# Kernel tuning notes

Measured on AMD Instinct MI355X. Metric: run time of the kernel, lower is better.

Reference implementation:

```python
import jax, jax.numpy as jnp
from jax import lax
import numpy as np

TOP_K = 2
CAPACITY_FACTOR = 1.0


def setup_inputs() -> dict:
    key = jax.random.key(0)
    kx, kg, k1, k2 = jax.random.split(key, 4)
    B, S, D, F, E = 8, 4096, 512, 1024, 16
    x = jax.random.normal(kx, (B, S, D), dtype=jnp.float32)
    w_gate = jax.random.normal(kg, (D, E), dtype=jnp.float32) * 0.02
    w1 = jax.random.normal(k1, (E, D, 2 * F), dtype=jnp.float32) * 0.02
    w2 = jax.random.normal(k2, (E, F, D), dtype=jnp.float32) * 0.02
    return {"x": x, "w_gate": w_gate, "w1": w1, "w2": w2}


def reference(x, w_gate, w1, w2):
    # Inference mode: no gating noise, dropout is identity.
    B, S, D = x.shape
    E = w_gate.shape[1]
    T = B * S
    capacity = max(1, int(CAPACITY_FACTOR * T / E))  # static

    flat = x.reshape(T, D)
    gate_logits = flat @ w_gate                      # [T, E]
    gate_scores = jax.nn.softmax(gate_logits, axis=-1)
    topk_vals, topk_idx = lax.top_k(gate_scores, TOP_K)  # [T, k]

    phi_mean = gate_scores.mean(axis=0)
    aux_loss = E * jnp.sum(phi_mean * phi_mean)

    # Per-expert combine weight for every token: [E, T]
    onehot = topk_idx[None, :, :] == jnp.arange(E)[:, None, None]  # [E, T, k]
    w_et = jnp.sum(jnp.where(onehot, topk_vals[None], 0.0), axis=-1)  # [E, T]

    # Capacity truncation: keep the `capacity` highest-weight tokens per expert
    sel_w, sel_idx = lax.top_k(w_et, capacity)  # [E, C]; unrouted picks have weight 0

    xs = flat[sel_idx]                                  # [E, C, D] gather
    h = jnp.einsum('ecd,edf->ecf', xs, w1)              # [E, C, 2F]
    h1, h2 = jnp.split(h, 2, axis=-1)
    act = h1 * jax.nn.silu(h2)                          # SwiGLU
    out_e = jnp.einsum('ecf,efd->ecd', act, w2) * sel_w[..., None]  # [E, C, D]

    combined = jnp.zeros((T, D), dtype=flat.dtype).at[sel_idx.reshape(-1)].add(
        out_e.reshape(-1, D))
    return combined.reshape(B, S, D), aux_loss
```

## Files before the change

### kernel.cpp

```cpp
#include <hip/hip_runtime.h>
#include <hip/hip_bf16.h>
#include <math.h>

#define T_TOK 32768
#define D_DIM 512
#define E_EXP 16
#define F_DIM 1024
#define C_CAP 2048

typedef __attribute__((ext_vector_type(8))) __bf16 bf16x8;
typedef __attribute__((ext_vector_type(4))) float f32x4;

__device__ __forceinline__ unsigned short f2bf(float f) {
  unsigned u = __float_as_uint(f);
  u += 0x7FFFu + ((u >> 16) & 1u);
  return (unsigned short)(u >> 16);
}

__device__ __forceinline__ void gld16(const void* gptr, void* ldsptr) {
  __builtin_amdgcn_global_load_lds(
      (__attribute__((address_space(1))) void*)(void*)gptr,
      (__attribute__((address_space(3))) void*)ldsptr, 16, 0, 0);
}

__global__ void transpose_conv_kernel(const float* __restrict__ in,
                                      unsigned short* __restrict__ out,
                                      int R, int Cc) {
  __shared__ float tile[32][33];
  int e = blockIdx.z;
  int r0 = blockIdx.y * 32, c0 = blockIdx.x * 32;
  const float* pin = in + (size_t)e * R * Cc;
  unsigned short* pout = out + (size_t)e * R * Cc;
  int tx = threadIdx.x, ty = threadIdx.y;
  #pragma unroll
  for (int i = 0; i < 32; i += 8)
    tile[ty + i][tx] = pin[(size_t)(r0 + ty + i) * Cc + c0 + tx];
  __syncthreads();
  #pragma unroll
  for (int i = 0; i < 32; i += 8)
    pout[(size_t)(c0 + ty + i) * R + r0 + tx] = f2bf(tile[tx][ty + i]);
}

__global__ __launch_bounds__(256) void gate_kernel(
    const float* __restrict__ x, const float* __restrict__ wg,
    float* __restrict__ w_et, float* __restrict__ phi_sum,
    unsigned short* __restrict__ xb) {
  __shared__ float wgl[D_DIM * E_EXP];
  __shared__ float phil[E_EXP];
  int tid = threadIdx.x;
  for (int i = tid; i < D_DIM * E_EXP; i += 256) wgl[i] = wg[i];
  if (tid < E_EXP) phil[tid] = 0.f;
  __syncthreads();

  int g = tid >> 4;
  int e = tid & 15;
  int t = blockIdx.x * 16 + g;

  float acc = 0.f;
  const float* xr = x + (size_t)t * D_DIM;
  #pragma unroll 4
  for (int d = 0; d < D_DIM; d += 4) {
    float4 xv = *(const float4*)(xr + d);
    acc = fmaf(xv.x, wgl[(d + 0) * 16 + e], acc);
    acc = fmaf(xv.y, wgl[(d + 1) * 16 + e], acc);
    acc = fmaf(xv.z, wgl[(d + 2) * 16 + e], acc);
    acc = fmaf(xv.w, wgl[(d + 3) * 16 + e], acc);
  }

  unsigned short* xrow = xb + (size_t)t * D_DIM;
  #pragma unroll
  for (int j = 0; j < 8; ++j) {
    int idx = j * 16 + e;
    float4 v = *(const float4*)(xr + idx * 4);
    ushort4 o;
    o.x = f2bf(v.x); o.y = f2bf(v.y); o.z = f2bf(v.z); o.w = f2bf(v.w);
    ((ushort4*)xrow)[idx] = o;
  }

  float m = acc;
  for (int off = 8; off; off >>= 1) m = fmaxf(m, __shfl_xor(m, off));
  float p = expf(acc - m);
  float s = p;
  for (int off = 8; off; off >>= 1) s += __shfl_xor(s, off);
  float score = p / s;
  atomicAdd(&phil[e], score);

  float v1 = score; int i1 = e;
  for (int off = 8; off; off >>= 1) {
    float ov = __shfl_xor(v1, off); int oi = __shfl_xor(i1, off);
    if (ov > v1 || (ov == v1 && oi < i1)) { v1 = ov; i1 = oi; }
  }
  float sc2 = (e == i1) ? -1.f : score;
  float v2 = sc2; int i2 = e;
  for (int off = 8; off; off >>= 1) {
    float ov = __shfl_xor(v2, off); int oi = __shfl_xor(i2, off);
    if (ov > v2 || (ov == v2 && oi < i2)) { v2 = ov; i2 = oi; }
  }
  if (e == 0) {
    w_et[(size_t)i1 * T_TOK + t] = v1;
    w_et[(size_t)i2 * T_TOK + t] = v2;
  }
  __syncthreads();
  if (tid < E_EXP) atomicAdd(&phi_sum[tid], phil[tid]);
}

__global__ void aux_kernel(const float* __restrict__ phi_sum, float* __restrict__ out_aux) {
  if (threadIdx.x == 0) {
    float s = 0.f;
    for (int e = 0; e < E_EXP; ++e) {
      float pm = phi_sum[e] / (float)T_TOK;
      s += pm * pm;
    }
    *out_aux = (float)E_EXP * s;
  }
}

template<int P>
__global__ __launch_bounds__(256) void s_hist(
    const float* __restrict__ w_et, unsigned* __restrict__ hist,
    const unsigned* __restrict__ prefix, const unsigned* __restrict__ done) {
  int c = blockIdx.x, e = blockIdx.y, tid = threadIdx.x;
  if (P > 0 && done[e]) return;
  __shared__ unsigned lh[2048];
  for (int i = tid; i < 2048; i += 256) lh[i] = 0;
  __syncthreads();
  const float* w = w_et + (size_t)e * T_TOK + c * 2048;
  unsigned pfx = (P > 0) ? prefix[e] : 0u;
  #pragma unroll
  for (int i = 0; i < 8; ++i) {
    unsigned b = __float_as_uint(w[i * 256 + tid]);
    if (P == 0) { if (b) atomicAdd(&lh[b >> 21], 1u); }
    else if (P == 1) { if ((b >> 21) == (pfx >> 21)) atomicAdd(&lh[(b >> 10) & 0x7FFu], 1u); }
    else { if ((b >> 10) == (pfx >> 10)) atomicAdd(&lh[b & 0x3FFu], 1u); }
  }
  __syncthreads();
  for (int i = tid; i < 2048; i += 256)
    if (lh[i]) atomicAdd(&hist[e * 2048 + i], lh[i]);
}

template<int P>
__global__ __launch_bounds__(1024) void s_pick(
    const unsigned* __restrict__ hist, unsigned* __restrict__ prefix,
    unsigned* __restrict__ krem, unsigned* __restrict__ done) {
  int tid = threadIdx.x, lane = tid & 63, e = tid >> 6;
  if (P > 0 && done[e]) return;
  const int BPL = (P == 2) ? 16 : 32;
  const int SH = (P == 0) ? 21 : (P == 1) ? 10 : 0;
  const unsigned* h = hist + e * 2048;
  unsigned S = 0;
  for (int i = 0; i < BPL; ++i) S += h[lane * BPL + i];
  unsigned U = S;
  #pragma unroll
  for (int off = 1; off < 64; off <<= 1) {
    unsigned t = __shfl_down(U, off);
    if (lane + off < 64) U += t;
  }
  unsigned Unext = __shfl_down(U, 1);
  if (lane == 63) Unext = 0;
  unsigned k = (P == 0) ? (unsigned)C_CAP : krem[e];
  if (P == 0 && lane == 0) {
    if (U < k) { done[e] = 1; prefix[e] = 0; krem[e] = 0; }
    else done[e] = 0;
  }
  if (U >= k && Unext < k) {
    unsigned cum = Unext; int chosen = 0; unsigned knew = 0;
    for (int i = BPL - 1; i >= 0; --i) {
      unsigned hh = h[lane * BPL + i];
      if (cum + hh >= k) { chosen = lane * BPL + i; knew = k - cum; break; }
      cum += hh;
    }
    if (P == 0) prefix[e] = ((unsigned)chosen) << SH;
    else prefix[e] = prefix[e] | (((unsigned)chosen) << SH);
    krem[e] = knew;
  }
}

__global__ __launch_bounds__(256) void s_count(
    const float* __restrict__ w_et, const unsigned* __restrict__ prefix,
    unsigned* __restrict__ cnt) {
  int c = blockIdx.x, e = blockIdx.y, tid = threadIdx.x;
  unsigned thr = prefix[e];
  const uint4* up = (const uint4*)(w_et + (size_t)e * T_TOK + c * 2048 + tid * 8);
  uint4 va = up[0], vb = up[1];
  unsigned gt = 0, eq = 0;
  unsigned vals[8] = {va.x, va.y, va.z, va.w, vb.x, vb.y, vb.z, vb.w};
  #pragma unroll
  for (int i = 0; i < 8; ++i) {
    if (vals[i] > thr) gt++;
    else if (vals[i] == thr) eq++;
  }
  __shared__ unsigned sc[256];
  sc[tid] = (gt << 16) | eq;
  __syncthreads();
  for (int s = 128; s; s >>= 1) {
    if (tid < s) sc[tid] += sc[tid + s];
    __syncthreads();
  }
  if (tid == 0) cnt[e * 16 + c] = sc[0];
}

__global__ __launch_bounds__(64) void s_base(
    const unsigned* __restrict__ cnt, unsigned* __restrict__ gbase,
    unsigned* __restrict__ ebase, unsigned* __restrict__ gtt,
    unsigned* __restrict__ eqt) {
  int e = threadIdx.x;
  if (e >= 16) return;
  unsigned g = 0, q = 0;
  #pragma unroll
  for (int c = 0; c < 16; ++c) {
    unsigned p = cnt[e * 16 + c];
    gbase[e * 16 + c] = g;
    ebase[e * 16 + c] = q;
    g += p >> 16;
    q += p & 0xFFFFu;
  }
  gtt[e] = g;
  eqt[e] = (unsigned)C_CAP - g;
}

__global__ __launch_bounds__(256) void s_write(
    const float* __restrict__ w_et, const unsigned* __restrict__ prefix,
    const unsigned* __restrict__ gbase, const unsigned* __restrict__ ebase,
    const unsigned* __restrict__ gtt, const unsigned* __restrict__ eqt,
    int* __restrict__ sel_idx, float* __restrict__ sel_w) {
  int c = blockIdx.x, e = blockIdx.y, tid = threadIdx.x;
  unsigned thr = prefix[e];
  const uint4* up = (const uint4*)(w_et + (size_t)e * T_TOK + c * 2048 + tid * 8);
  uint4 va = up[0], vb = up[1];
  unsigned vals[8] = {va.x, va.y, va.z, va.w, vb.x, vb.y, vb.z, vb.w};
  unsigned gt = 0, eq = 0;
  #pragma unroll
  for (int i = 0; i < 8; ++i) {
    if (vals[i] > thr) gt++;
    else if (vals[i] == thr) eq++;
  }
  __shared__ unsigned sc[256];
  unsigned mine = (gt << 16) | eq;
  sc[tid] = mine;
  __syncthreads();
  for (int off = 1; off < 256; off <<= 1) {
    unsigned add = (tid >= off) ? sc[tid - off] : 0u;
    __syncthreads();
    sc[tid] += add;
    __syncthreads();
  }
  unsigned excl = sc[tid] - mine;
  unsigned gpos = gbase[e * 16 + c] + (excl >> 16);
  unsigned qpos = ebase[e * 16 + c] + (excl & 0xFFFFu);
  unsigned gtotal = gtt[e], eqtake = eqt[e];
  int* si = sel_idx + (size_t)e * C_CAP;
  float* sw = sel_w + (size_t)e * C_CAP;
  int tokbase = c * 2048 + tid * 8;
  #pragma unroll
  for (int i = 0; i < 8; ++i) {
    unsigned b = vals[i];
    if (b > thr) {
      si[gpos] = tokbase + i; sw[gpos] = __uint_as_float(b); gpos++;
    } else if (b == thr && qpos < eqtake) {
      si[gtotal + qpos] = tokbase + i; sw[gtotal + qpos] = __uint_as_float(b); qpos++;
    }
  }
}


#define PIPE_BARRIER() do { __builtin_amdgcn_s_barrier(); __builtin_amdgcn_sched_barrier(0); } while (0)

__global__ __launch_bounds__(256, 3) void gemm1_kernel(
    const unsigned short* __restrict__ xb,
    const unsigned short* __restrict__ w1t,
    const int* __restrict__ sel_idx,
    unsigned short* __restrict__ act) {
  __shared__ __align__(16) unsigned short As[3 * 4096];
  __shared__ __align__(16) unsigned short Bs[3 * 4096];
  int bid = (blockIdx.x & 7) * 512 + (blockIdx.x >> 3);
  int nt = bid & 15, mt = (bid >> 4) & 15, e = bid >> 8;
  int tid = threadIdx.x, lane = tid & 63, wid = tid >> 6;
  int wr = wid >> 1, wc = wid & 1;
  int cl = lane & 15, rg = lane >> 4;

  int c0 = tid, c1 = 256 + tid;
  int r0 = c0 >> 2, gk0 = (c0 & 3) ^ ((r0 >> 1) & 3);
  int r1 = c1 >> 2, gk1 = (c1 & 3) ^ ((r1 >> 1) & 3);
  int tok0 = sel_idx[e * C_CAP + mt * 128 + r0];
  int tok1 = sel_idx[e * C_CAP + mt * 128 + r1];
  const unsigned short* ag0 = xb + (size_t)tok0 * D_DIM + gk0 * 8;
  const unsigned short* ag1 = xb + (size_t)tok1 * D_DIM + gk1 * 8;
  int hcol0 = (r0 < 64) ? (nt * 64 + r0) : (F_DIM + nt * 64 + (r0 - 64));
  int hcol1 = (r1 < 64) ? (nt * 64 + r1) : (F_DIM + nt * 64 + (r1 - 64));
  const unsigned short* bg0 = w1t + ((size_t)e * 2 * F_DIM + hcol0) * D_DIM + gk0 * 8;
  const unsigned short* bg1 = w1t + ((size_t)e * 2 * F_DIM + hcol1) * D_DIM + gk1 * 8;
  char* Ab = (char*)As;
  char* Bb = (char*)Bs;

#define G1_STAGE(buf, kt) do { \
    gld16(ag0 + (kt) * 32, Ab + (buf) * 8192 + tid * 16); \
    gld16(ag1 + (kt) * 32, Ab + (buf) * 8192 + 4096 + tid * 16); \
    gld16(bg0 + (kt) * 32, Bb + (buf) * 8192 + tid * 16); \
    gld16(bg1 + (kt) * 32, Bb + (buf) * 8192 + 4096 + tid * 16); \
  } while (0)

  f32x4 zero = {0.f, 0.f, 0.f, 0.f};
  f32x4 acc[4][4];
  #pragma unroll
  for (int m = 0; m < 4; ++m)
    #pragma unroll
    for (int n = 0; n < 4; ++n) acc[m][n] = zero;

#define G1_COMPUTE(buf) do { \
    const unsigned short* Ap = As + (buf) * 4096; \
    const unsigned short* Bp = Bs + (buf) * 4096; \
    bf16x8 av[4], bv[4]; \
    _Pragma("unroll") \
    for (int m = 0; m < 4; ++m) { \
      int ra = wr * 64 + m * 16 + cl; \
      av[m] = *(const bf16x8*)&Ap[(ra * 4 + (rg ^ ((ra >> 1) & 3))) * 8]; \
    } \
    _Pragma("unroll") \
    for (int n = 0; n < 4; ++n) { \
      int rb = ((n < 2) ? (wc * 32 + n * 16) : (64 + wc * 32 + (n - 2) * 16)) + cl; \
      bv[n] = *(const bf16x8*)&Bp[(rb * 4 + (rg ^ ((rb >> 1) & 3))) * 8]; \
    } \
    _Pragma("unroll") \
    for (int m = 0; m < 4; ++m) \
      _Pragma("unroll") \
      for (int n = 0; n < 4; ++n) \
        acc[m][n] = __builtin_amdgcn_mfma_f32_16x16x32_bf16(av[m], bv[n], acc[m][n], 0, 0, 0); \
  } while (0)

  const int NK = D_DIM / 32;
  G1_STAGE(0, 0);
  G1_STAGE(1, 1);
  int bc = 0, bs = 2;
  for (int kt = 0; kt < NK - 1; ++kt) {
    asm volatile("s_waitcnt vmcnt(4)" ::: "memory");
    PIPE_BARRIER();
    if (kt + 2 < NK) { G1_STAGE(bs, kt + 2); bs = (bs == 2) ? 0 : bs + 1; }
    __builtin_amdgcn_sched_barrier(0);
    G1_COMPUTE(bc);
    bc = (bc == 2) ? 0 : bc + 1;
  }
  asm volatile("s_waitcnt vmcnt(0)" ::: "memory");
  PIPE_BARRIER();
  G1_COMPUTE(bc);

  #pragma unroll
  for (int m = 0; m < 4; ++m) {
    #pragma unroll
    for (int n = 0; n < 2; ++n) {
      #pragma unroll
      for (int r = 0; r < 4; ++r) {
        int row = mt * 128 + wr * 64 + m * 16 + rg * 4 + r;
        int col = nt * 64 + wc * 32 + n * 16 + cl;
        float h1 = acc[m][n][r];
        float h2 = acc[m][n + 2][r];
        float sg = h2 / (1.f + __expf(-h2));
        act[((size_t)e * C_CAP + row) * F_DIM + col] = f2bf(h1 * sg);
      }
    }
  }
#undef G1_STAGE
#undef G1_COMPUTE
}

__global__ __launch_bounds__(256, 3) void gemm2_kernel(
    const unsigned short* __restrict__ act,
    const unsigned short* __restrict__ w2t,
    const int* __restrict__ sel_idx,
    const float* __restrict__ sel_w,
    float* __restrict__ out) {
  __shared__ __align__(16) unsigned short As[3 * 4096];
  __shared__ __align__(16) unsigned short Bs[3 * 4096];
  int bid = (blockIdx.x & 7) * 128 + (blockIdx.x >> 3);
  int nt = bid & 3, mt = (bid >> 2) & 15, e = bid >> 6;
  int tid = threadIdx.x, lane = tid & 63, wid = tid >> 6;
  int wr = wid >> 1, wc = wid & 1;
  int cl = lane & 15, rg = lane >> 4;

  int c0 = tid, c1 = 256 + tid;
  int r0 = c0 >> 2, gk0 = (c0 & 3) ^ ((r0 >> 1) & 3);
  int r1 = c1 >> 2, gk1 = (c1 & 3) ^ ((r1 >> 1) & 3);
  const unsigned short* ag0 = act + ((size_t)e * C_CAP + mt * 128 + r0) * F_DIM + gk0 * 8;
  const unsigned short* ag1 = act + ((size_t)e * C_CAP + mt * 128 + r1) * F_DIM + gk1 * 8;
  const unsigned short* bg0 = w2t + ((size_t)e * D_DIM + nt * 128 + r0) * F_DIM + gk0 * 8;
  const unsigned short* bg1 = w2t + ((size_t)e * D_DIM + nt * 128 + r1) * F_DIM + gk1 * 8;
  char* Ab = (char*)As;
  char* Bb = (char*)Bs;

#define G2_STAGE(buf, kt) do { \
    gld16(ag0 + (kt) * 32, Ab + (buf) * 8192 + tid * 16); \
    gld16(ag1 + (kt) * 32, Ab + (buf) * 8192 + 4096 + tid * 16); \
    gld16(bg0 + (kt) * 32, Bb + (buf) * 8192 + tid * 16); \
    gld16(bg1 + (kt) * 32, Bb + (buf) * 8192 + 4096 + tid * 16); \
  } while (0)

  f32x4 zero = {0.f, 0.f, 0.f, 0.f};
  f32x4 acc[4][4];
  #pragma unroll
  for (int m = 0; m < 4; ++m)
    #pragma unroll
    for (int n = 0; n < 4; ++n) acc[m][n] = zero;

#define G2_COMPUTE(buf) do { \
    const unsigned short* Ap = As + (buf) * 4096; \
    const unsigned short* Bp = Bs + (buf) * 4096; \
    bf16x8 av[4], bv[4]; \
    _Pragma("unroll") \
    for (int m = 0; m < 4; ++m) { \
      int ra = wr * 64 + m * 16 + cl; \
      av[m] = *(const bf16x8*)&Ap[(ra * 4 + (rg ^ ((ra >> 1) & 3))) * 8]; \
    } \
    _Pragma("unroll") \
    for (int n = 0; n < 4; ++n) { \
      int rb = wc * 64 + n * 16 + cl; \
      bv[n] = *(const bf16x8*)&Bp[(rb * 4 + (rg ^ ((rb >> 1) & 3))) * 8]; \
    } \
    _Pragma("unroll") \
    for (int m = 0; m < 4; ++m) \
      _Pragma("unroll") \
      for (int n = 0; n < 4; ++n) \
        acc[m][n] = __builtin_amdgcn_mfma_f32_16x16x32_bf16(av[m], bv[n], acc[m][n], 0, 0, 0); \
  } while (0)

  const int NK = F_DIM / 32;
  G2_STAGE(0, 0);
  G2_STAGE(1, 1);
  int bc = 0, bs = 2;
  for (int kt = 0; kt < NK - 1; ++kt) {
    asm volatile("s_waitcnt vmcnt(4)" ::: "memory");
    PIPE_BARRIER();
    if (kt + 2 < NK) { G2_STAGE(bs, kt + 2); bs = (bs == 2) ? 0 : bs + 1; }
    __builtin_amdgcn_sched_barrier(0);
    G2_COMPUTE(bc);
    bc = (bc == 2) ? 0 : bc + 1;
  }
  asm volatile("s_waitcnt vmcnt(0)" ::: "memory");
  PIPE_BARRIER();
  G2_COMPUTE(bc);

  #pragma unroll
  for (int m = 0; m < 4; ++m) {
    #pragma unroll
    for (int r = 0; r < 4; ++r) {
      int slot = mt * 128 + wr * 64 + m * 16 + rg * 4 + r;
      float wgt = sel_w[e * C_CAP + slot];
      int tok = sel_idx[e * C_CAP + slot];
      float* orow = out + (size_t)tok * D_DIM;
      #pragma unroll
      for (int n = 0; n < 4; ++n) {
        int col = nt * 128 + wc * 64 + n * 16 + cl;
        atomicAdd(&orow[col], acc[m][n][r] * wgt);
      }
    }
  }
#undef G2_STAGE
#undef G2_COMPUTE
}

extern "C" void kernel_launch(void* const* d_in, const int* in_sizes, int n_in,
                              void* d_out, int out_size, void* d_ws, size_t ws_size,
                              hipStream_t stream) {
  const float* x  = (const float*)d_in[0];
  const float* wg = (const float*)d_in[1];
  const float* w1 = (const float*)d_in[2];
  const float* w2 = (const float*)d_in[3];
  float* out = (float*)d_out;

  char* ws = (char*)d_ws;
  size_t off = 0;
  auto carve = [&](size_t bytes) -> void* {
    void* p = ws + off;
    off += (bytes + 255) & ~(size_t)255;
    return p;
  };
  float* w_et            = (float*)carve((size_t)E_EXP * T_TOK * 4);
  float* phi             = (float*)carve(64);
  int* sel_i             = (int*)carve((size_t)E_EXP * C_CAP * 4);
  float* sel_wv          = (float*)carve((size_t)E_EXP * C_CAP * 4);
  unsigned short* xb     = (unsigned short*)carve((size_t)T_TOK * D_DIM * 2);
  unsigned short* w1t    = (unsigned short*)carve((size_t)E_EXP * 2 * F_DIM * D_DIM * 2);
  unsigned short* w2t    = (unsigned short*)carve((size_t)E_EXP * D_DIM * F_DIM * 2);
  unsigned short* actb   = (unsigned short*)carve((size_t)E_EXP * C_CAP * F_DIM * 2);
  unsigned* hist0        = (unsigned*)carve((size_t)E_EXP * 2048 * 4);
  unsigned* hist1        = (unsigned*)carve((size_t)E_EXP * 2048 * 4);
  unsigned* hist2        = (unsigned*)carve((size_t)E_EXP * 2048 * 4);
  unsigned* prefix       = (unsigned*)carve(64 * 4);
  unsigned* krem         = (unsigned*)carve(64 * 4);
  unsigned* done         = (unsigned*)carve(64 * 4);
  unsigned* cnt          = (unsigned*)carve(256 * 4);
  unsigned* gbase        = (unsigned*)carve(256 * 4);
  unsigned* ebase        = (unsigned*)carve(256 * 4);
  unsigned* gtt          = (unsigned*)carve(64 * 4);
  unsigned* eqt          = (unsigned*)carve(64 * 4);
  if (off > ws_size) return;

  hipMemsetAsync(w_et, 0, (size_t)E_EXP * T_TOK * 4, stream);
  hipMemsetAsync(phi, 0, 64, stream);
  hipMemsetAsync(hist0, 0, (size_t)E_EXP * 2048 * 4 * 3, stream);
  hipMemsetAsync(d_out, 0, (size_t)out_size * 4, stream);

  transpose_conv_kernel<<<dim3(2 * F_DIM / 32, D_DIM / 32, E_EXP), dim3(32, 8), 0, stream>>>(
      w1, w1t, D_DIM, 2 * F_DIM);
  transpose_conv_kernel<<<dim3(D_DIM / 32, F_DIM / 32, E_EXP), dim3(32, 8), 0, stream>>>(
      w2, w2t, F_DIM, D_DIM);
  gate_kernel<<<T_TOK / 16, 256, 0, stream>>>(x, wg, w_et, phi, xb);

  s_hist<0><<<dim3(16, 16), 256, 0, stream>>>(w_et, hist0, prefix, done);
  s_pick<0><<<1, 1024, 0, stream>>>(hist0, prefix, krem, done);
  s_hist<1><<<dim3(16, 16), 256, 0, stream>>>(w_et, hist1, prefix, done);
  s_pick<1><<<1, 1024, 0, stream>>>(hist1, prefix, krem, done);
  s_hist<2><<<dim3(16, 16), 256, 0, stream>>>(w_et, hist2, prefix, done);
  s_pick<2><<<1, 1024, 0, stream>>>(hist2, prefix, krem, done);
  s_count<<<dim3(16, 16), 256, 0, stream>>>(w_et, prefix, cnt);
  s_base<<<1, 64, 0, stream>>>(cnt, gbase, ebase, gtt, eqt);
  s_write<<<dim3(16, 16), 256, 0, stream>>>(w_et, prefix, gbase, ebase, gtt, eqt,
                                            sel_i, sel_wv);

  aux_kernel<<<1, 64, 0, stream>>>(phi, out + (size_t)T_TOK * D_DIM);
  gemm1_kernel<<<E_EXP * 16 * 16, 256, 0, stream>>>(xb, w1t, sel_i, actb);
  gemm2_kernel<<<E_EXP * 16 * 4, 256, 0, stream>>>(actb, w2t, sel_i, sel_wv, out);
}
```

Before: 336.4 us.

## Deepen GEMM pipelines to five stages, add setprio, fold s_base into s_write

Both expert GEMMs move from a 3-buffer to a 5-buffer LDS ring with four tiles prefetched ahead, and the waitcnt thresholds and loop tail change to match. Occupancy drops from 3 to 2 blocks per CU. s_setprio raises wave priority around the MFMA bursts. The separate s_base launch is removed: each s_write block computes its own prefix offsets from cnt in shared memory, saving one tiny kernel launch. The deeper prefetch is meant to hide global-load latency better, but the larger LDS footprint and lower occupancy may cancel that.

```diff
diff --git a/kernel.cpp b/kernel.cpp
--- a/kernel.cpp
+++ b/kernel.cpp
@@ -199,32 +199,23 @@
   if (tid == 0) cnt[e * 16 + c] = sc[0];
 }
 
-__global__ __launch_bounds__(64) void s_base(
-    const unsigned* __restrict__ cnt, unsigned* __restrict__ gbase,
-    unsigned* __restrict__ ebase, unsigned* __restrict__ gtt,
-    unsigned* __restrict__ eqt) {
-  int e = threadIdx.x;
-  if (e >= 16) return;
-  unsigned g = 0, q = 0;
-  #pragma unroll
-  for (int c = 0; c < 16; ++c) {
-    unsigned p = cnt[e * 16 + c];
-    gbase[e * 16 + c] = g;
-    ebase[e * 16 + c] = q;
-    g += p >> 16;
-    q += p & 0xFFFFu;
-  }
-  gtt[e] = g;
-  eqt[e] = (unsigned)C_CAP - g;
-}
-
 __global__ __launch_bounds__(256) void s_write(
     const float* __restrict__ w_et, const unsigned* __restrict__ prefix,
-    const unsigned* __restrict__ gbase, const unsigned* __restrict__ ebase,
-    const unsigned* __restrict__ gtt, const unsigned* __restrict__ eqt,
+    const unsigned* __restrict__ cnt,
     int* __restrict__ sel_idx, float* __restrict__ sel_w) {
   int c = blockIdx.x, e = blockIdx.y, tid = threadIdx.x;
   unsigned thr = prefix[e];
+  __shared__ unsigned s_gb, s_eb, s_gt, s_eq;
+  if (tid == 0) {
+    unsigned g = 0, q = 0, gb = 0, eb = 0;
+    #pragma unroll
+    for (int c2 = 0; c2 < 16; ++c2) {
+      unsigned p = cnt[e * 16 + c2];
+      if (c2 < c) { gb += p >> 16; eb += p & 0xFFFFu; }
+      g += p >> 16; q += p & 0xFFFFu;
+    }
+    s_gb = gb; s_eb = eb; s_gt = g; s_eq = (unsigned)C_CAP - g;
+  }
   const uint4* up = (const uint4*)(w_et + (size_t)e * T_TOK + c * 2048 + tid * 8);
   uint4 va = up[0], vb = up[1];
   unsigned vals[8] = {va.x, va.y, va.z, va.w, vb.x, vb.y, vb.z, vb.w};
@@ -245,9 +236,9 @@
     __syncthreads();
   }
   unsigned excl = sc[tid] - mine;
-  unsigned gpos = gbase[e * 16 + c] + (excl >> 16);
-  unsigned qpos = ebase[e * 16 + c] + (excl & 0xFFFFu);
-  unsigned gtotal = gtt[e], eqtake = eqt[e];
+  unsigned gpos = s_gb + (excl >> 16);
+  unsigned qpos = s_eb + (excl & 0xFFFFu);
+  unsigned gtotal = s_gt, eqtake = s_eq;
   int* si = sel_idx + (size_t)e * C_CAP;
   float* sw = sel_w + (size_t)e * C_CAP;
   int tokbase = c * 2048 + tid * 8;
@@ -265,13 +256,13 @@
 
 #define PIPE_BARRIER() do { __builtin_amdgcn_s_barrier(); __builtin_amdgcn_sched_barrier(0); } while (0)
 
-__global__ __launch_bounds__(256, 3) void gemm1_kernel(
+__global__ __launch_bounds__(256, 2) void gemm1_kernel(
     const unsigned short* __restrict__ xb,
     const unsigned short* __restrict__ w1t,
     const int* __restrict__ sel_idx,
     unsigned short* __restrict__ act) {
-  __shared__ __align__(16) unsigned short As[3 * 4096];
-  __shared__ __align__(16) unsigned short Bs[3 * 4096];
+  __shared__ __align__(16) unsigned short As[5 * 4096];
+  __shared__ __align__(16) unsigned short Bs[5 * 4096];
   int bid = (blockIdx.x & 7) * 512 + (blockIdx.x >> 3);
   int nt = bid & 15, mt = (bid >> 4) & 15, e = bid >> 8;
   int tid = threadIdx.x, lane = tid & 63, wid = tid >> 6;
@@ -320,25 +311,36 @@
       int rb = ((n < 2) ? (wc * 32 + n * 16) : (64 + wc * 32 + (n - 2) * 16)) + cl; \
       bv[n] = *(const bf16x8*)&Bp[(rb * 4 + (rg ^ ((rb >> 1) & 3))) * 8]; \
     } \
+    __builtin_amdgcn_s_setprio(1); \
     _Pragma("unroll") \
     for (int m = 0; m < 4; ++m) \
       _Pragma("unroll") \
       for (int n = 0; n < 4; ++n) \
         acc[m][n] = __builtin_amdgcn_mfma_f32_16x16x32_bf16(av[m], bv[n], acc[m][n], 0, 0, 0); \
+    __builtin_amdgcn_s_setprio(0); \
   } while (0)
 
   const int NK = D_DIM / 32;
-  G1_STAGE(0, 0);
-  G1_STAGE(1, 1);
-  int bc = 0, bs = 2;
-  for (int kt = 0; kt < NK - 1; ++kt) {
-    asm volatile("s_waitcnt vmcnt(4)" ::: "memory");
+  G1_STAGE(0, 0); G1_STAGE(1, 1); G1_STAGE(2, 2); G1_STAGE(3, 3);
+  int bc = 0, bs = 4;
+  for (int kt = 0; kt < NK - 4; ++kt) {
+    asm volatile("s_waitcnt vmcnt(12)" ::: "memory");
     PIPE_BARRIER();
-    if (kt + 2 < NK) { G1_STAGE(bs, kt + 2); bs = (bs == 2) ? 0 : bs + 1; }
+    G1_STAGE(bs, kt + 4);
+    bs = (bs == 4) ? 0 : bs + 1;
     __builtin_amdgcn_sched_barrier(0);
     G1_COMPUTE(bc);
-    bc = (bc == 2) ? 0 : bc + 1;
-  }
+    bc = (bc == 4) ? 0 : bc + 1;
+  }
+  asm volatile("s_waitcnt vmcnt(12)" ::: "memory");
+  PIPE_BARRIER();
+  G1_COMPUTE(bc); bc = (bc == 4) ? 0 : bc + 1;
+  asm volatile("s_waitcnt vmcnt(8)" ::: "memory");
+  PIPE_BARRIER();
+  G1_COMPUTE(bc); bc = (bc == 4) ? 0 : bc + 1;
+  asm volatile("s_waitcnt vmcnt(4)" ::: "memory");
+  PIPE_BARRIER();
+  G1_COMPUTE(bc); bc = (bc == 4) ? 0 : bc + 1;
   asm volatile("s_waitcnt vmcnt(0)" ::: "memory");
   PIPE_BARRIER();
   G1_COMPUTE(bc);
@@ -362,14 +364,14 @@
 #undef G1_COMPUTE
 }
 
-__global__ __launch_bounds__(256, 3) void gemm2_kernel(
+__global__ __launch_bounds__(256, 2) void gemm2_kernel(
     const unsigned short* __restrict__ act,
     const unsigned short* __restrict__ w2t,
     const int* __restrict__ sel_idx,
     const float* __restrict__ sel_w,
     float* __restrict__ out) {
-  __shared__ __align__(16) unsigned short As[3 * 4096];
-  __shared__ __align__(16) unsigned short Bs[3 * 4096];
+  __shared__ __align__(16) unsigned short As[5 * 4096];
+  __shared__ __align__(16) unsigned short Bs[5 * 4096];
   int bid = (blockIdx.x & 7) * 128 + (blockIdx.x >> 3);
   int nt = bid & 3, mt = (bid >> 2) & 15, e = bid >> 6;
   int tid = threadIdx.x, lane = tid & 63, wid = tid >> 6;
@@ -414,25 +416,36 @@
       int rb = wc * 64 + n * 16 + cl; \
       bv[n] = *(const bf16x8*)&Bp[(rb * 4 + (rg ^ ((rb >> 1) & 3))) * 8]; \
     } \
+    __builtin_amdgcn_s_setprio(1); \
     _Pragma("unroll") \
     for (int m = 0; m < 4; ++m) \
       _Pragma("unroll") \
       for (int n = 0; n < 4; ++n) \
         acc[m][n] = __builtin_amdgcn_mfma_f32_16x16x32_bf16(av[m], bv[n], acc[m][n], 0, 0, 0); \
+    __builtin_amdgcn_s_setprio(0); \
   } while (0)
 
   const int NK = F_DIM / 32;
-  G2_STAGE(0, 0);
-  G2_STAGE(1, 1);
-  int bc = 0, bs = 2;
-  for (int kt = 0; kt < NK - 1; ++kt) {
-    asm volatile("s_waitcnt vmcnt(4)" ::: "memory");
+  G2_STAGE(0, 0); G2_STAGE(1, 1); G2_STAGE(2, 2); G2_STAGE(3, 3);
+  int bc = 0, bs = 4;
+  for (int kt = 0; kt < NK - 4; ++kt) {
+    asm volatile("s_waitcnt vmcnt(12)" ::: "memory");
     PIPE_BARRIER();
-    if (kt + 2 < NK) { G2_STAGE(bs, kt + 2); bs = (bs == 2) ? 0 : bs + 1; }
+    G2_STAGE(bs, kt + 4);
+    bs = (bs == 4) ? 0 : bs + 1;
     __builtin_amdgcn_sched_barrier(0);
     G2_COMPUTE(bc);
-    bc = (bc == 2) ? 0 : bc + 1;
-  }
+    bc = (bc == 4) ? 0 : bc + 1;
+  }
+  asm volatile("s_waitcnt vmcnt(12)" ::: "memory");
+  PIPE_BARRIER();
+  G2_COMPUTE(bc); bc = (bc == 4) ? 0 : bc + 1;
+  asm volatile("s_waitcnt vmcnt(8)" ::: "memory");
+  PIPE_BARRIER();
+  G2_COMPUTE(bc); bc = (bc == 4) ? 0 : bc + 1;
+  asm volatile("s_waitcnt vmcnt(4)" ::: "memory");
+  PIPE_BARRIER();
+  G2_COMPUTE(bc); bc = (bc == 4) ? 0 : bc + 1;
   asm volatile("s_waitcnt vmcnt(0)" ::: "memory");
   PIPE_BARRIER();
   G2_COMPUTE(bc);
@@ -487,10 +500,6 @@
   unsigned* krem         = (unsigned*)carve(64 * 4);
   unsigned* done         = (unsigned*)carve(64 * 4);
   unsigned* cnt          = (unsigned*)carve(256 * 4);
-  unsigned* gbase        = (unsigned*)carve(256 * 4);
-  unsigned* ebase        = (unsigned*)carve(256 * 4);
-  unsigned* gtt          = (unsigned*)carve(64 * 4);
-  unsigned* eqt          = (unsigned*)carve(64 * 4);
   if (off > ws_size) return;
 
   hipMemsetAsync(w_et, 0, (size_t)E_EXP * T_TOK * 4, stream);
@@ -511,9 +520,7 @@
   s_hist<2><<<dim3(16, 16), 256, 0, stream>>>(w_et, hist2, prefix, done);
   s_pick<2><<<1, 1024, 0, stream>>>(hist2, prefix, krem, done);
   s_count<<<dim3(16, 16), 256, 0, stream>>>(w_et, prefix, cnt);
-  s_base<<<1, 64, 0, stream>>>(cnt, gbase, ebase, gtt, eqt);
-  s_write<<<dim3(16, 16), 256, 0, stream>>>(w_et, prefix, gbase, ebase, gtt, eqt,
-                                            sel_i, sel_wv);
+  s_write<<<dim3(16, 16), 256, 0, stream>>>(w_et, prefix, cnt, sel_i, sel_wv);
 
   aux_kernel<<<1, 64, 0, stream>>>(phi, out + (size_t)T_TOK * D_DIM);
   gemm1_kernel<<<E_EXP * 16 * 16, 256, 0, stream>>>(xb, w1t, sel_i, actb);
```

Result: no change. 341.6 us (+1.6%).
